# Kernel optimization log

Hardware: AMD Instinct MI355X
Metric: run time of the kernel (lower is better)

Reference implementation:

```python
import jax, jax.numpy as jnp
import numpy as np

BETA = 0.25


def setup_inputs() -> dict:
    key = jax.random.key(0)
    k1, k2 = jax.random.split(key)
    inputs = jax.random.normal(k1, (32, 4096, 64), dtype=jnp.float32)
    # VarianceScaling(uniform) ~ small-magnitude init; plain normal scaled works for a numeric reference
    codebook = jax.random.normal(k2, (1024, 64), dtype=jnp.float32) * (1.0 / np.sqrt(64.0))
    return {"inputs": inputs, "codebook": codebook}


def reference(inputs, codebook):
    D = codebook.shape[-1]
    flat = jnp.reshape(inputs, (-1, D))                      # [N, D]
    flat_sqr = jnp.sum(flat ** 2, axis=-1, keepdims=True)    # [N, 1]
    code_sqr = jnp.sum(codebook ** 2, axis=-1)[None, :]      # [1, K]
    # full pairwise squared distances [N, K]
    distances = flat_sqr - 2.0 * (flat @ codebook.T) + code_sqr
    encoding_indices = jnp.reshape(jnp.argmin(distances, axis=-1), inputs.shape[:-1])
    quantize = codebook[encoding_indices]                    # gather -> [..., D]
    encoding_loss = jnp.mean((jax.lax.stop_gradient(inputs) - quantize) ** 2)
    commit_loss = jnp.mean((inputs - jax.lax.stop_gradient(quantize)) ** 2)
    loss = encoding_loss + BETA * commit_loss
    # straight-through estimator
    z_q = inputs + jax.lax.stop_gradient(quantize - inputs)
    return loss, z_q, encoding_indices
```

## Files before the change

### kernel.cpp

```cpp
#include <hip/hip_runtime.h>

#define N_ROWS 131072
#define D 64
#define K_CODES 1024

typedef _Float16 f16x8 __attribute__((ext_vector_type(8)));
typedef float    f32x4 __attribute__((ext_vector_type(4)));

#define MFMA16(a, b, c) __builtin_amdgcn_mfma_f32_16x16x32_f16((a), (b), (c), 0, 0, 0)

__global__ __launch_bounds__(256)
void prep_kernel(const float* __restrict__ CB, _Float16* __restrict__ CBf,
                 float* __restrict__ csqr, float* __restrict__ loss) {
    const int b = blockIdx.x, t = threadIdx.x;
    if (b < 64) {
        const int unit = b * 256 + t;
        const int tile = unit >> 8;
        const int f    = (unit >> 6) & 3;
        const int lane = unit & 63;
        const int quad = lane >> 4, lrow = lane & 15;
        const int code = tile * 16 + lrow;
        const int k0   = (f & 1) * 32 + quad * 8;
        const float* src = CB + (size_t)code * D + k0;
        float4 v0 = *(const float4*)(src);
        float4 v1 = *(const float4*)(src + 4);
        float xs[8] = {v0.x, v0.y, v0.z, v0.w, v1.x, v1.y, v1.z, v1.w};
        f16x8 o;
#pragma unroll
        for (int j = 0; j < 8; ++j) {
            float sv = -2.0f * xs[j];
            _Float16 h = (_Float16)sv;
            o[j] = (f < 2) ? h : (_Float16)(sv - (float)h);
        }
        *(f16x8*)(CBf + (size_t)unit * 8) = o;
    } else {
        if (t == 0) *loss = 0.0f;
        for (int k = t; k < K_CODES; k += 256) {
            const float4* p = (const float4*)(CB + (size_t)k * D);
            float s = 0.0f;
#pragma unroll
            for (int i = 0; i < 16; ++i) {
                float4 v = p[i];
                s += v.x * v.x + v.y * v.y + v.z * v.z + v.w * v.w;
            }
            csqr[k] = s;
        }
    }
}

__device__ __forceinline__ void gload_lds16(const void* g, void* l) {
    __builtin_amdgcn_global_load_lds(
        (const __attribute__((address_space(1))) void*)g,
        (__attribute__((address_space(3))) void*)l,
        16, 0, 0);
}

__global__ __launch_bounds__(256, 4)
void argmin_kernel(const float* __restrict__ X,
                   const _Float16* __restrict__ CBf,
                   const float* __restrict__ csqr,
                   const float* __restrict__ CB,
                   float* __restrict__ out) {
    __shared__ _Float16 Bring[2][4][2048];
    __shared__ float LsC[K_CODES];
    __shared__ int   ivfin[128];
    __shared__ float lsum[4];

    const int t    = threadIdx.x;
    const int wave = t >> 6;
    const int lane = t & 63;
    const int quad = lane >> 4;
    const int lrow = lane & 15;
    const int R0   = blockIdx.x * 128;
    const int Rw   = R0 + wave * 32;

#define STAGE(g_, buf_)                                                       \
    do {                                                                      \
        _Pragma("unroll")                                                     \
        for (int i_ = 0; i_ < 4; ++i_) {                                      \
            const f16x8* gp_ =                                                \
                (const f16x8*)CBf + (size_t)((g_) * 4 + i_) * 256 + t;        \
            gload_lds16((const void*)gp_,                                     \
                        (void*)((char*)&Bring[buf_][i_][0] + (wave << 10)));  \
        }                                                                     \
    } while (0)

#define READB(Bv, i_)                                                         \
    do {                                                                      \
        const f16x8* Bt_ = (const f16x8*)(Bb + (i_) * 2048) + lane;           \
        Bv[0] = Bt_[0];                                                       \
        Bv[1] = Bt_[64];                                                      \
        Bv[2] = Bt_[128];                                                     \
        Bv[3] = Bt_[192];                                                     \
    } while (0)

#define TILECOMP(Bv, i_)                                                      \
    do {                                                                      \
        const int   c_  = (g * 4 + (i_)) * 16 + lrow;                         \
        const float cs_ = LsC[c_];                                            \
        _Pragma("unroll")                                                     \
        for (int mt = 0; mt < 2; ++mt) {                                      \
            f32x4 acc = {cs_, cs_, cs_, cs_};                                 \
            acc = MFMA16(Ah[mt][0], Bv[0], acc);                              \
            acc = MFMA16(Ah[mt][1], Bv[1], acc);                              \
            acc = MFMA16(Al[mt][0], Bv[0], acc);                              \
            acc = MFMA16(Al[mt][1], Bv[1], acc);                              \
            acc = MFMA16(Ah[mt][0], Bv[2], acc);                              \
            acc = MFMA16(Ah[mt][1], Bv[3], acc);                              \
            _Pragma("unroll")                                                 \
            for (int r = 0; r < 4; ++r) {                                     \
                bool lt = acc[r] < bestd[mt][r];                              \
                bestd[mt][r] = lt ? acc[r] : bestd[mt][r];                    \
                besti[mt][r] = lt ? c_ : besti[mt][r];                        \
            }                                                                 \
        }                                                                     \
    } while (0)

#define CONSUME()                                                             \
    do {                                                                      \
        f16x8 B0[4], B1[4];                                                   \
        READB(B0, 0);                                                         \
        READB(B1, 1);                                                         \
        TILECOMP(B0, 0);                                                      \
        READB(B0, 2);                                                         \
        TILECOMP(B1, 1);                                                      \
        READB(B1, 3);                                                         \
        TILECOMP(B0, 2);                                                      \
        TILECOMP(B1, 3);                                                      \
    } while (0)

    STAGE(0, 0);

    ((float4*)LsC)[t] = ((const float4*)csqr)[t];

    f16x8 Ah[2][2], Al[2][2];
    float xsq = 0.0f;
#pragma unroll
    for (int mt = 0; mt < 2; ++mt) {
        const float* xr = X + (size_t)(Rw + mt * 16 + lrow) * D;
#pragma unroll
        for (int ks = 0; ks < 2; ++ks) {
            const int k0 = ks * 32 + quad * 8;
            float4 v0 = *(const float4*)(xr + k0);
            float4 v1 = *(const float4*)(xr + k0 + 4);
            float xs[8] = {v0.x, v0.y, v0.z, v0.w, v1.x, v1.y, v1.z, v1.w};
            f16x8 h, l;
#pragma unroll
            for (int j = 0; j < 8; ++j) {
                xsq += xs[j] * xs[j];
                _Float16 hh = (_Float16)xs[j];
                h[j] = hh;
                l[j] = (_Float16)(xs[j] - (float)hh);
            }
            Ah[mt][ks] = h;
            Al[mt][ks] = l;
        }
    }

    float bestd[2][4];
    int   besti[2][4];
#pragma unroll
    for (int mt = 0; mt < 2; ++mt)
#pragma unroll
        for (int r = 0; r < 4; ++r) { bestd[mt][r] = 3.0e38f; besti[mt][r] = 0; }

    __syncthreads();

    {
        const int g = 0;
        STAGE(1, 1);
        const _Float16* Bb = &Bring[0][0][0];
        CONSUME();
    }
    for (int g = 1; g < 16; ++g) {
        asm volatile("s_waitcnt vmcnt(0)" ::: "memory");
        __builtin_amdgcn_s_barrier();
        if (g < 15) STAGE(g + 1, (g + 1) & 1);
        const _Float16* Bb = &Bring[g & 1][0][0];
        CONSUME();
    }

    float dvsum = 0.0f;
#pragma unroll
    for (int mt = 0; mt < 2; ++mt) {
#pragma unroll
        for (int r = 0; r < 4; ++r) {
            float dv = bestd[mt][r];
            int   iv = besti[mt][r];
#pragma unroll
            for (int m = 1; m < 16; m <<= 1) {
                float od = __shfl_xor(dv, m, 64);
                int   oi = __shfl_xor(iv, m, 64);
                if (od < dv || (od == dv && oi < iv)) { dv = od; iv = oi; }
            }
            if (lrow == 0) {
                const int rl = wave * 32 + mt * 16 + quad * 4 + r;
                ivfin[rl] = iv;
                out[1 + (size_t)N_ROWS * D + R0 + rl] = (float)iv;
                dvsum += dv;
            }
        }
    }

    {
        float s = xsq + dvsum;
#pragma unroll
        for (int m = 1; m < 64; m <<= 1) s += __shfl_xor(s, m, 64);
        if (lane == 0) lsum[wave] = s;
    }
    __syncthreads();

    const float scale = 1.25f / (float)((size_t)N_ROWS * D);
    if (t == 0)
        atomicAdd(out, (lsum[0] + lsum[1] + lsum[2] + lsum[3]) * scale);

    float* p = out + 1 + (size_t)R0 * D;
#pragma unroll
    for (int i = 0; i < 8; ++i) {
        int q = i * 256 + t;
        int j = 4 * q + 3;
        if (q < 2047) {
            float v[4];
#pragma unroll
            for (int e = 0; e < 4; ++e) {
                int jj = j + e;
                v[e] = CB[(size_t)ivfin[jj >> 6] * D + (jj & 63)];
            }
            *(float4*)(p + j) = make_float4(v[0], v[1], v[2], v[3]);
        } else if (q == 2047) {
            p[8191] = CB[(size_t)ivfin[127] * D + 63];
        }
    }
    if (t == 0) {
        const float* c0 = CB + (size_t)ivfin[0] * D;
        p[0] = c0[0];
        p[1] = c0[1];
        p[2] = c0[2];
    }
}

extern "C" void kernel_launch(void* const* d_in, const int* in_sizes, int n_in,
                              void* d_out, int out_size, void* d_ws,
                              size_t ws_size, hipStream_t stream) {
    const float* X  = (const float*)d_in[0];
    const float* CB = (const float*)d_in[1];

    float*    csqr = (float*)d_ws;
    _Float16* CBf  = (_Float16*)((char*)d_ws + 4096);

    hipLaunchKernelGGL(prep_kernel, dim3(65), dim3(256), 0, stream,
                       CB, CBf, csqr, (float*)d_out);
    hipLaunchKernelGGL(argmin_kernel, dim3(N_ROWS / 128), dim3(256), 0, stream,
                       X, CBf, csqr, CB, (float*)d_out);
}
```

Baseline: 145.0 us.

## Switch distance GEMM to 32x32x16 MFMA tiles with relaid codebook

Replaces the 16x16x32 f16 MFMA tiling with 32x32x16 MFMA, so each wave computes a 32-row by 32-code tile per instruction group. The codebook preparation layout, LDS staging layout and argmin reduction (now over 32 lanes, 16 accumulator slots) are reworked to match. The aim is fewer MFMA issues and fewer B-fragment LDS reads per distance. The cost is larger accumulators (16 floats plus 16 indices per lane), which raises register pressure and may hurt occupancy. The tree reduction also grows to five shuffle steps per slot across 16 slots.

Measured after the change: 158.6 us. 1.09x slower.

```diff
diff --git a/kernel.cpp b/kernel.cpp
--- a/kernel.cpp
+++ b/kernel.cpp
@@ -4,10 +4,10 @@
 #define D 64
 #define K_CODES 1024
 
-typedef _Float16 f16x8 __attribute__((ext_vector_type(8)));
-typedef float    f32x4 __attribute__((ext_vector_type(4)));
-
-#define MFMA16(a, b, c) __builtin_amdgcn_mfma_f32_16x16x32_f16((a), (b), (c), 0, 0, 0)
+typedef _Float16 f16x8  __attribute__((ext_vector_type(8)));
+typedef float    f32x16 __attribute__((ext_vector_type(16)));
+
+#define MFMA32(a, b, c) __builtin_amdgcn_mfma_f32_32x32x16_f16((a), (b), (c), 0, 0, 0)
 
 __global__ __launch_bounds__(256)
 void prep_kernel(const float* __restrict__ CB, _Float16* __restrict__ CBf,
@@ -15,12 +15,12 @@
     const int b = blockIdx.x, t = threadIdx.x;
     if (b < 64) {
         const int unit = b * 256 + t;
-        const int tile = unit >> 8;
-        const int f    = (unit >> 6) & 3;
-        const int lane = unit & 63;
-        const int quad = lane >> 4, lrow = lane & 15;
-        const int code = tile * 16 + lrow;
-        const int k0   = (f & 1) * 32 + quad * 8;
+        const int tile = unit >> 9;
+        const int rem  = unit & 511;
+        const int f    = rem >> 6;
+        const int lane = rem & 63;
+        const int code = tile * 32 + (lane & 31);
+        const int k0   = (f & 3) * 16 + (lane >> 5) * 8;
         const float* src = CB + (size_t)code * D + k0;
         float4 v0 = *(const float4*)(src);
         float4 v1 = *(const float4*)(src + 4);
@@ -30,7 +30,7 @@
         for (int j = 0; j < 8; ++j) {
             float sv = -2.0f * xs[j];
             _Float16 h = (_Float16)sv;
-            o[j] = (f < 2) ? h : (_Float16)(sv - (float)h);
+            o[j] = (f < 4) ? h : (_Float16)(sv - (float)h);
         }
         *(f16x8*)(CBf + (size_t)unit * 8) = o;
     } else {
@@ -61,7 +61,7 @@
                    const float* __restrict__ csqr,
                    const float* __restrict__ CB,
                    float* __restrict__ out) {
-    __shared__ _Float16 Bring[2][4][2048];
+    __shared__ _Float16 Bring[2][2][4096];
     __shared__ float LsC[K_CODES];
     __shared__ int   ivfin[128];
     __shared__ float lsum[4];
@@ -69,8 +69,8 @@
     const int t    = threadIdx.x;
     const int wave = t >> 6;
     const int lane = t & 63;
-    const int quad = lane >> 4;
-    const int lrow = lane & 15;
+    const int col  = lane & 31;
+    const int hi5  = lane >> 5;
     const int R0   = blockIdx.x * 128;
     const int Rw   = R0 + wave * 32;
 
@@ -78,69 +78,25 @@
     do {                                                                      \
         _Pragma("unroll")                                                     \
         for (int i_ = 0; i_ < 4; ++i_) {                                      \
+            const int u_ = i_ * 256 + t;                                      \
             const f16x8* gp_ =                                                \
-                (const f16x8*)CBf + (size_t)((g_) * 4 + i_) * 256 + t;        \
+                (const f16x8*)CBf + (size_t)((g_) * 1024 + u_);               \
             gload_lds16((const void*)gp_,                                     \
-                        (void*)((char*)&Bring[buf_][i_][0] + (wave << 10)));  \
+                        (void*)((char*)&Bring[buf_][0][0] + (size_t)u_ * 16));\
         }                                                                     \
     } while (0)
 
-#define READB(Bv, i_)                                                         \
-    do {                                                                      \
-        const f16x8* Bt_ = (const f16x8*)(Bb + (i_) * 2048) + lane;           \
-        Bv[0] = Bt_[0];                                                       \
-        Bv[1] = Bt_[64];                                                      \
-        Bv[2] = Bt_[128];                                                     \
-        Bv[3] = Bt_[192];                                                     \
-    } while (0)
-
-#define TILECOMP(Bv, i_)                                                      \
-    do {                                                                      \
-        const int   c_  = (g * 4 + (i_)) * 16 + lrow;                         \
-        const float cs_ = LsC[c_];                                            \
-        _Pragma("unroll")                                                     \
-        for (int mt = 0; mt < 2; ++mt) {                                      \
-            f32x4 acc = {cs_, cs_, cs_, cs_};                                 \
-            acc = MFMA16(Ah[mt][0], Bv[0], acc);                              \
-            acc = MFMA16(Ah[mt][1], Bv[1], acc);                              \
-            acc = MFMA16(Al[mt][0], Bv[0], acc);                              \
-            acc = MFMA16(Al[mt][1], Bv[1], acc);                              \
-            acc = MFMA16(Ah[mt][0], Bv[2], acc);                              \
-            acc = MFMA16(Ah[mt][1], Bv[3], acc);                              \
-            _Pragma("unroll")                                                 \
-            for (int r = 0; r < 4; ++r) {                                     \
-                bool lt = acc[r] < bestd[mt][r];                              \
-                bestd[mt][r] = lt ? acc[r] : bestd[mt][r];                    \
-                besti[mt][r] = lt ? c_ : besti[mt][r];                        \
-            }                                                                 \
-        }                                                                     \
-    } while (0)
-
-#define CONSUME()                                                             \
-    do {                                                                      \
-        f16x8 B0[4], B1[4];                                                   \
-        READB(B0, 0);                                                         \
-        READB(B1, 1);                                                         \
-        TILECOMP(B0, 0);                                                      \
-        READB(B0, 2);                                                         \
-        TILECOMP(B1, 1);                                                      \
-        READB(B1, 3);                                                         \
-        TILECOMP(B0, 2);                                                      \
-        TILECOMP(B1, 3);                                                      \
-    } while (0)
-
     STAGE(0, 0);
 
     ((float4*)LsC)[t] = ((const float4*)csqr)[t];
 
-    f16x8 Ah[2][2], Al[2][2];
+    f16x8 Ah[4], Al[4];
     float xsq = 0.0f;
-#pragma unroll
-    for (int mt = 0; mt < 2; ++mt) {
-        const float* xr = X + (size_t)(Rw + mt * 16 + lrow) * D;
-#pragma unroll
-        for (int ks = 0; ks < 2; ++ks) {
-            const int k0 = ks * 32 + quad * 8;
+    {
+        const float* xr = X + (size_t)(Rw + col) * D;
+#pragma unroll
+        for (int c = 0; c < 4; ++c) {
+            const int k0 = c * 16 + hi5 * 8;
             float4 v0 = *(const float4*)(xr + k0);
             float4 v1 = *(const float4*)(xr + k0 + 4);
             float xs[8] = {v0.x, v0.y, v0.z, v0.w, v1.x, v1.y, v1.z, v1.w};
@@ -152,53 +108,77 @@
                 h[j] = hh;
                 l[j] = (_Float16)(xs[j] - (float)hh);
             }
-            Ah[mt][ks] = h;
-            Al[mt][ks] = l;
-        }
-    }
-
-    float bestd[2][4];
-    int   besti[2][4];
-#pragma unroll
-    for (int mt = 0; mt < 2; ++mt)
-#pragma unroll
-        for (int r = 0; r < 4; ++r) { bestd[mt][r] = 3.0e38f; besti[mt][r] = 0; }
+            Ah[c] = h;
+            Al[c] = l;
+        }
+    }
+
+    float bestd[16];
+    int   besti[16];
+#pragma unroll
+    for (int s = 0; s < 16; ++s) { bestd[s] = 3.0e38f; besti[s] = 0; }
+
+#define TILECOMP(i_)                                                          \
+    do {                                                                      \
+        const f16x8* Bt_ = (const f16x8*)&Bring[g & 1][i_][0];                \
+        const int   T_  = g * 2 + (i_);                                       \
+        const int   ci_ = T_ * 32 + col;                                      \
+        const float cs_ = LsC[ci_];                                           \
+        f16x8 bh[4], bl[4];                                                   \
+        _Pragma("unroll")                                                     \
+        for (int c = 0; c < 4; ++c) bh[c] = Bt_[c * 64 + lane];               \
+        _Pragma("unroll")                                                     \
+        for (int c = 0; c < 4; ++c) bl[c] = Bt_[(4 + c) * 64 + lane];         \
+        f32x16 acc;                                                           \
+        _Pragma("unroll")                                                     \
+        for (int s = 0; s < 16; ++s) acc[s] = cs_;                            \
+        _Pragma("unroll")                                                     \
+        for (int c = 0; c < 4; ++c) acc = MFMA32(Ah[c], bh[c], acc);          \
+        _Pragma("unroll")                                                     \
+        for (int c = 0; c < 4; ++c) acc = MFMA32(Al[c], bh[c], acc);          \
+        _Pragma("unroll")                                                     \
+        for (int c = 0; c < 4; ++c) acc = MFMA32(Ah[c], bl[c], acc);          \
+        _Pragma("unroll")                                                     \
+        for (int s = 0; s < 16; ++s) {                                        \
+            bool lt = acc[s] < bestd[s];                                      \
+            bestd[s] = lt ? acc[s] : bestd[s];                                \
+            besti[s] = lt ? ci_ : besti[s];                                   \
+        }                                                                     \
+    } while (0)
 
     __syncthreads();
 
     {
         const int g = 0;
         STAGE(1, 1);
-        const _Float16* Bb = &Bring[0][0][0];
-        CONSUME();
+        TILECOMP(0);
+        TILECOMP(1);
     }
     for (int g = 1; g < 16; ++g) {
         asm volatile("s_waitcnt vmcnt(0)" ::: "memory");
         __builtin_amdgcn_s_barrier();
         if (g < 15) STAGE(g + 1, (g + 1) & 1);
-        const _Float16* Bb = &Bring[g & 1][0][0];
-        CONSUME();
+        TILECOMP(0);
+        TILECOMP(1);
     }
 
     float dvsum = 0.0f;
 #pragma unroll
-    for (int mt = 0; mt < 2; ++mt) {
-#pragma unroll
-        for (int r = 0; r < 4; ++r) {
-            float dv = bestd[mt][r];
-            int   iv = besti[mt][r];
-#pragma unroll
-            for (int m = 1; m < 16; m <<= 1) {
-                float od = __shfl_xor(dv, m, 64);
-                int   oi = __shfl_xor(iv, m, 64);
-                if (od < dv || (od == dv && oi < iv)) { dv = od; iv = oi; }
-            }
-            if (lrow == 0) {
-                const int rl = wave * 32 + mt * 16 + quad * 4 + r;
-                ivfin[rl] = iv;
-                out[1 + (size_t)N_ROWS * D + R0 + rl] = (float)iv;
-                dvsum += dv;
-            }
+    for (int s = 0; s < 16; ++s) {
+        float dv = bestd[s];
+        int   iv = besti[s];
+#pragma unroll
+        for (int m = 1; m < 32; m <<= 1) {
+            float od = __shfl_xor(dv, m, 64);
+            int   oi = __shfl_xor(iv, m, 64);
+            if (od < dv || (od == dv && oi < iv)) { dv = od; iv = oi; }
+        }
+        if (col == 0) {
+            const int r  = (s & 3) + 8 * (s >> 2) + 4 * hi5;
+            const int rl = wave * 32 + r;
+            ivfin[rl] = iv;
+            out[1 + (size_t)N_ROWS * D + R0 + rl] = (float)iv;
+            dvsum += dv;
         }
     }
 
```
